# Optimization experiments

Hardware: AMD Instinct MI355X
Metric: run time of the kernel (lower is better)

## Reference

```python
import jax, jax.numpy as jnp
import numpy as np


def _dequantize_and_unpack(packed, scales):
    """packed: [d_out, d_in//2] int8, each byte holds two 4-bit nibbles.
    Returns [d_out, d_in] in scales.dtype, scaled per output row."""
    low = (packed & 15).astype(jnp.int8)
    high = (packed >> 4).astype(jnp.int8)  # arithmetic shift, like torch int8 >> 4
    low = jnp.where(low > 7, low - 16, low)
    high = jnp.where(high > 7, high - 16, high)
    # interleave: even cols = high nibble, odd cols = low nibble
    w = jnp.stack([high, low], axis=-1).reshape(packed.shape[0], -1)
    return w.astype(scales.dtype) * scales


def setup_inputs() -> dict:
    key = jax.random.key(0)
    ks = jax.random.split(key, 7)
    d = 4096
    N = 4096
    x = jax.random.normal(ks[0], (N, d), dtype=jnp.float32)
    fc1_weights_packed = jax.random.randint(ks[1], (2 * d, d // 2), -8, 7, dtype=jnp.int32).astype(jnp.int8)
    fc1_scales = (jax.random.normal(ks[2], (2 * d, 1), dtype=jnp.float32) * 0.02).astype(jnp.float16)
    fc1_bias = jax.random.normal(ks[3], (2 * d,), dtype=jnp.float32)
    fc2_weights_packed = jax.random.randint(ks[4], (d, d), -8, 7, dtype=jnp.int32).astype(jnp.int8)
    fc2_scales = (jax.random.normal(ks[5], (d, 1), dtype=jnp.float32) * 0.02).astype(jnp.float16)
    fc2_bias = jax.random.normal(ks[6], (d,), dtype=jnp.float32)
    return {
        "x": x,
        "fc1_weights_packed": fc1_weights_packed,
        "fc1_scales": fc1_scales,
        "fc1_bias": fc1_bias,
        "fc2_weights_packed": fc2_weights_packed,
        "fc2_scales": fc2_scales,
        "fc2_bias": fc2_bias,
    }


def reference(x, fc1_weights_packed, fc1_scales, fc1_bias,
              fc2_weights_packed, fc2_scales, fc2_bias):
    # fc1: dequantize to [2d, d], linear, relu
    w1 = _dequantize_and_unpack(fc1_weights_packed, fc1_scales).astype(x.dtype)
    h = jax.nn.relu(jnp.dot(x, w1.T) + fc1_bias)
    # fc2: dequantize to [d, 2d], linear
    w2 = _dequantize_and_unpack(fc2_weights_packed, fc2_scales).astype(x.dtype)
    return jnp.dot(h, w2.T) + fc2_bias
```

## Files before the change

kernel.cpp:

```cpp
#include <hip/hip_runtime.h>
#include <hip/hip_fp16.h>
#include <stdint.h>


typedef __attribute__((ext_vector_type(4)))  int i32x4;
typedef __attribute__((ext_vector_type(16))) int i32x16;
typedef __attribute__((ext_vector_type(8))) _Float16 f16x8;

__device__ __forceinline__ void load_lds16(const void* g, void* l) {
    __builtin_amdgcn_global_load_lds(
        (__attribute__((address_space(1))) void*)(void*)g,
        (__attribute__((address_space(3))) void*)(void*)l,
        16, 0, 0);
}

__device__ __forceinline__ float block_max(float m, int tid) {
    __shared__ float red[4];
#pragma unroll
    for (int off = 32; off; off >>= 1)
        m = fmaxf(m, __shfl_down(m, off, 64));
    if ((tid & 63) == 0) red[tid >> 6] = m;
    __syncthreads();
    m = fmaxf(fmaxf(red[0], red[1]), fmaxf(red[2], red[3]));
    __syncthreads();
    return m;
}

__global__ __launch_bounds__(256) void quant_x(
    const float* __restrict__ in, int* __restrict__ out,
    float* __restrict__ rscale, int ncols)
{
    const int tid = threadIdx.x;
    const int row = blockIdx.x;
    const float4* rp = (const float4*)(in + (size_t)row * ncols);
    const int nf4 = ncols / 4;
    float4 v[4];
    float m = 0.f;
#pragma unroll
    for (int k = 0; k < 4; ++k) {
        v[k] = rp[k * 256 + tid];
        m = fmaxf(m, fmaxf(fmaxf(fabsf(v[k].x), fabsf(v[k].y)),
                           fmaxf(fabsf(v[k].z), fabsf(v[k].w))));
    }
    m = block_max(m, tid);
    m = fmaxf(m, 1e-20f);
    const float inv = 127.f / m;
    if (tid == 0) rscale[row] = m / 127.f;
    int* orow = out + (size_t)row * nf4;
#pragma unroll
    for (int k = 0; k < 4; ++k) {
        int q0 = __float2int_rn(v[k].x * inv);
        int q1 = __float2int_rn(v[k].y * inv);
        int q2 = __float2int_rn(v[k].z * inv);
        int q3 = __float2int_rn(v[k].w * inv);
        orow[k * 256 + tid] = (q0 & 0xFF) | ((q1 & 0xFF) << 8) |
                              ((q2 & 0xFF) << 16) | ((q3 & 0xFF) << 24);
    }
}

__global__ __launch_bounds__(256) void quant_h(
    const _Float16* __restrict__ in, int2* __restrict__ out,
    float* __restrict__ rscale, int ncols)
{
    const int tid = threadIdx.x;
    const int row = blockIdx.x;
    const f16x8* rp = (const f16x8*)(in + (size_t)row * ncols);
    const int nv = ncols / 8;
    f16x8 v[4];
    float m = 0.f;
#pragma unroll
    for (int k = 0; k < 4; ++k) {
        v[k] = rp[k * 256 + tid];
#pragma unroll
        for (int e = 0; e < 8; ++e) m = fmaxf(m, (float)v[k][e]);
    }
    m = block_max(m, tid);
    m = fmaxf(m, 1e-20f);
    const float inv = 255.f / m;
    if (tid == 0) rscale[row] = m / 255.f;
    int2* orow = out + (size_t)row * nv;
#pragma unroll
    for (int k = 0; k < 4; ++k) {
        union { int8_t b[8]; int2 w; } u;
#pragma unroll
        for (int e = 0; e < 8; ++e) {
            int q = __float2int_rn((float)v[k][e] * inv);
            q = q < 0 ? 0 : (q > 255 ? 255 : q);
            u.b[e] = (int8_t)(q - 128);
        }
        orow[k * 256 + tid] = u.w;
    }
}

__global__ __launch_bounds__(256) void expand_int4_i8(
    const int4* __restrict__ packed, int2* __restrict__ out,
    int* __restrict__ wsum, int n_i4)
{
    const int tid = threadIdx.x;
    const int row = blockIdx.x;
    const int4* prow = packed + (size_t)row * n_i4;
    int2* orow = out + (size_t)row * n_i4;
    int sum = 0;
    for (int j = tid; j < n_i4; j += 256) {
        int4 p = prow[j];
        int vals[4] = {p.x, p.y, p.z, p.w};
        union { int8_t b[8]; int2 w; } u;
#pragma unroll
        for (int b = 0; b < 4; ++b) {
            int by = (int)(int8_t)(vals[b] & 0xFF);
            int hi = by >> 4;
            int lo = ((by & 15) ^ 8) - 8;
            u.b[2 * b] = (int8_t)hi;
            u.b[2 * b + 1] = (int8_t)lo;
            sum += hi + lo;
        }
        orow[j] = u.w;
    }
    __shared__ int sred[4];
#pragma unroll
    for (int off = 32; off; off >>= 1) sum += __shfl_down(sum, off, 64);
    if ((tid & 63) == 0) sred[tid >> 6] = sum;
    __syncthreads();
    if (tid == 0) wsum[row] = sred[0] + sred[1] + sred[2] + sred[3];
}

template <bool RELU, bool SHIFT, typename OutT>
__global__ __launch_bounds__(512, 2) void gemm_i8_256(
    const int8_t* __restrict__ A, const int8_t* __restrict__ B,
    OutT* __restrict__ C,
    const float* __restrict__ sa,
    const float* __restrict__ s,
    const float* __restrict__ bias,
    const int* __restrict__ wsum,
    int M, int N, int K)
{
    __shared__ alignas(16) char sA[2][256 * 128];
    __shared__ alignas(16) char sB[2][256 * 128];

    const int tid  = threadIdx.x;
    const int lane = tid & 63;
    const int wave = tid >> 6;
    const int wm = wave >> 2;
    const int wn = wave & 3;

    int bid = blockIdx.y * gridDim.x + blockIdx.x;
    const int xcd = bid & 7;
    const int idx = bid >> 3;
    const int cpx = gridDim.x >> 3;
    const int bx = xcd * cpx + idx / gridDim.y;
    const int by = idx % gridDim.y;
    const int bm = by * 256;
    const int bn = bx * 256;

    const int srow = tid >> 3;
    const int scol = ((tid & 7) ^ (srow & 7)) << 4;
    const int8_t* Ag = A + (size_t)(bm + srow) * K + scol;
    const int8_t* Bg = B + (size_t)(bn + srow) * K + scol;
    const size_t rK64 = (size_t)64 * K;
    const int ldst = tid * 16;

    auto stage_a = [&](int buf, int h, int kt) {
        const int8_t* g = Ag + (size_t)h * 128 * K + (size_t)kt * 128;
        char* l = &sA[buf][h * 16384 + ldst];
        load_lds16(g, l);
        load_lds16(g + rK64, l + 8192);
    };
    auto stage_b = [&](int buf, int h, int kt) {
        const int8_t* g = Bg + (size_t)h * 128 * K + (size_t)kt * 128;
        char* l = &sB[buf][h * 16384 + ldst];
        load_lds16(g, l);
        load_lds16(g + rK64, l + 8192);
    };

    const int l31 = lane & 31;
    const int kh  = lane >> 5;
    int coff[4];
#pragma unroll
    for (int ks = 0; ks < 4; ++ks)
        coff[ks] = (((ks * 2 + kh) ^ (l31 & 7)) << 4);
    int abase[4], bbase[2];
#pragma unroll
    for (int i = 0; i < 4; ++i) abase[i] = (wm * 128 + i * 32 + l31) * 128;
#pragma unroll
    for (int j = 0; j < 2; ++j) bbase[j] = (wn * 64 + j * 32 + l31) * 128;

    i32x16 acc[4][2] = {};
    const int NT = K >> 7;

    stage_a(0, 0, 0); stage_a(0, 1, 0);
    stage_b(0, 0, 0); stage_b(0, 1, 0);
    if (NT > 1) { stage_b(1, 0, 1); stage_b(1, 1, 1); }

#define MFMA_ROW(ri, AF)                                                   \
    do {                                                                   \
        __builtin_amdgcn_s_setprio(1);                                     \
        _Pragma("unroll")                                                  \
        for (int ks = 0; ks < 4; ++ks) {                                   \
            acc[ri][0] = __builtin_amdgcn_mfma_i32_32x32x32_i8(            \
                AF[ks], bf[0][ks], acc[ri][0], 0, 0, 0);                   \
            acc[ri][1] = __builtin_amdgcn_mfma_i32_32x32x32_i8(            \
                AF[ks], bf[1][ks], acc[ri][1], 0, 0, 0);                   \
        }                                                                  \
        __builtin_amdgcn_s_setprio(0);                                     \
    } while (0)

    for (int t = 0; t < NT; ++t) {
        const char* pA = sA[t & 1];
        const char* pB = sB[t & 1];
        if (t + 1 < NT) asm volatile("s_waitcnt vmcnt(4)" ::: "memory");
        else            asm volatile("s_waitcnt vmcnt(0)" ::: "memory");
        __builtin_amdgcn_s_barrier();
        __builtin_amdgcn_sched_barrier(0);

        i32x4 bf[2][4], afA[4], afB[4];
#pragma unroll
        for (int j = 0; j < 2; ++j)
#pragma unroll
            for (int ks = 0; ks < 4; ++ks)
                bf[j][ks] = *(const i32x4*)(pB + bbase[j] + coff[ks]);
#pragma unroll
        for (int ks = 0; ks < 4; ++ks)
            afA[ks] = *(const i32x4*)(pA + abase[0] + coff[ks]);
#pragma unroll
        for (int ks = 0; ks < 4; ++ks)
            afB[ks] = *(const i32x4*)(pA + abase[1] + coff[ks]);
        if (t + 1 < NT) stage_a((t + 1) & 1, 0, t + 1);
        __builtin_amdgcn_sched_barrier(0);
        asm volatile("s_waitcnt lgkmcnt(4)" ::: "memory");
        __builtin_amdgcn_sched_barrier(0);
        MFMA_ROW(0, afA);

#pragma unroll
        for (int ks = 0; ks < 4; ++ks)
            afA[ks] = *(const i32x4*)(pA + abase[2] + coff[ks]);
        if (t + 1 < NT) stage_a((t + 1) & 1, 1, t + 1);
        __builtin_amdgcn_sched_barrier(0);
        asm volatile("s_waitcnt lgkmcnt(4)" ::: "memory");
        __builtin_amdgcn_sched_barrier(0);
        MFMA_ROW(1, afB);

        __builtin_amdgcn_s_barrier();
        __builtin_amdgcn_sched_barrier(0);
#pragma unroll
        for (int ks = 0; ks < 4; ++ks)
            afB[ks] = *(const i32x4*)(pA + abase[3] + coff[ks]);
        if (t + 2 < NT) stage_b(t & 1, 0, t + 2);
        __builtin_amdgcn_sched_barrier(0);
        asm volatile("s_waitcnt lgkmcnt(4)" ::: "memory");
        __builtin_amdgcn_sched_barrier(0);
        MFMA_ROW(2, afA);

        if (t + 2 < NT) stage_b(t & 1, 1, t + 2);
        __builtin_amdgcn_sched_barrier(0);
        asm volatile("s_waitcnt lgkmcnt(0)" ::: "memory");
        __builtin_amdgcn_sched_barrier(0);
        MFMA_ROW(3, afB);
    }
#undef MFMA_ROW

#pragma unroll
    for (int j = 0; j < 2; ++j) {
        const int n  = bn + wn * 64 + j * 32 + l31;
        const float sc = s[n];
        const float bs = bias[n];
        const int shf = SHIFT ? 128 * wsum[n] : 0;
#pragma unroll
        for (int i = 0; i < 4; ++i) {
            const int mb = bm + wm * 128 + i * 32 + 4 * kh;
#pragma unroll
            for (int reg = 0; reg < 16; ++reg) {
                const int m = mb + (reg & 3) + 8 * (reg >> 2);
                float v = (float)(acc[i][j][reg] + shf) * sc * sa[m] + bs;
                if (RELU) v = v > 0.f ? v : 0.f;
                C[(size_t)m * N + n] = (OutT)v;
            }
        }
    }
}

extern "C" void kernel_launch(void* const* d_in, const int* in_sizes, int n_in,
                              void* d_out, int out_size, void* d_ws, size_t ws_size,
                              hipStream_t stream)
{
    const float* x   = (const float*)d_in[0];
    const int4*  w1p = (const int4*)d_in[1];
    const float* s1  = (const float*)d_in[2];
    const float* b1  = (const float*)d_in[3];
    const int4*  w2p = (const int4*)d_in[4];
    const float* s2  = (const float*)d_in[5];
    const float* b2  = (const float*)d_in[6];
    float* out = (float*)d_out;

    const int d    = in_sizes[6];
    const int d2   = in_sizes[3];
    const int Ntok = in_sizes[0] / d;

    char* ws = (char*)d_ws;
    int8_t*   xq = (int8_t*)ws;
    int8_t*   wq = (int8_t*)(ws + (size_t)Ntok * d);
    _Float16* hb = (_Float16*)(ws + (size_t)Ntok * d + (size_t)d2 * d);
    int8_t*   hq = (int8_t*)((char*)hb + (size_t)Ntok * d2 * 2);
    float*    sx = (float*)((char*)hq + (size_t)Ntok * d2);
    float*    sh = sx + Ntok;
    int*      wsum = (int*)(sh + Ntok);

    quant_x<<<Ntok, 256, 0, stream>>>(x, (int*)xq, sx, d);
    expand_int4_i8<<<d2, 256, 0, stream>>>(w1p, (int2*)wq, wsum, d / 8);
    {
        dim3 grid(d2 / 256, Ntok / 256);
        gemm_i8_256<true, false, _Float16><<<grid, 512, 0, stream>>>(
            xq, wq, hb, sx, s1, b1, nullptr, Ntok, d2, d);
    }
    quant_h<<<Ntok, 256, 0, stream>>>(hb, (int2*)hq, sh, d2);
    expand_int4_i8<<<d, 256, 0, stream>>>(w2p, (int2*)wq, wsum, d2 / 8);
    {
        dim3 grid(d / 256, Ntok / 256);
        gemm_i8_256<false, true, float><<<grid, 512, 0, stream>>>(
            hq, wq, out, sh, s2, b2, wsum, Ntok, d, d2);
    }
}
```

Baseline: 502.7 us.

## Reorder int8 GEMM main loop to iterate k-slices with double-buffered fragments

```diff
diff --git a/kernel.cpp b/kernel.cpp
--- a/kernel.cpp
+++ b/kernel.cpp
@@ -191,15 +191,25 @@
     stage_b(0, 0, 0); stage_b(0, 1, 0);
     if (NT > 1) { stage_b(1, 0, 1); stage_b(1, 1, 1); }
 
-#define MFMA_ROW(ri, AF)                                                   \
+#define READ_FRAGS(AF, BF, ks)                                             \
+    do {                                                                   \
+        _Pragma("unroll")                                                  \
+        for (int j = 0; j < 2; ++j)                                        \
+            BF[j] = *(const i32x4*)(pB + bbase[j] + coff[ks]);             \
+        _Pragma("unroll")                                                  \
+        for (int i = 0; i < 4; ++i)                                        \
+            AF[i] = *(const i32x4*)(pA + abase[i] + coff[ks]);             \
+    } while (0)
+
+#define MFMA8(AF, BF)                                                      \
     do {                                                                   \
         __builtin_amdgcn_s_setprio(1);                                     \
         _Pragma("unroll")                                                  \
-        for (int ks = 0; ks < 4; ++ks) {                                   \
-            acc[ri][0] = __builtin_amdgcn_mfma_i32_32x32x32_i8(            \
-                AF[ks], bf[0][ks], acc[ri][0], 0, 0, 0);                   \
-            acc[ri][1] = __builtin_amdgcn_mfma_i32_32x32x32_i8(            \
-                AF[ks], bf[1][ks], acc[ri][1], 0, 0, 0);                   \
+        for (int i = 0; i < 4; ++i) {                                      \
+            acc[i][0] = __builtin_amdgcn_mfma_i32_32x32x32_i8(             \
+                AF[i], BF[0], acc[i][0], 0, 0, 0);                         \
+            acc[i][1] = __builtin_amdgcn_mfma_i32_32x32x32_i8(             \
+                AF[i], BF[1], acc[i][1], 0, 0, 0);                         \
         }                                                                  \
         __builtin_amdgcn_s_setprio(0);                                     \
     } while (0)
@@ -212,51 +222,40 @@
         __builtin_amdgcn_s_barrier();
         __builtin_amdgcn_sched_barrier(0);
 
-        i32x4 bf[2][4], afA[4], afB[4];
-#pragma unroll
-        for (int j = 0; j < 2; ++j)
-#pragma unroll
-            for (int ks = 0; ks < 4; ++ks)
-                bf[j][ks] = *(const i32x4*)(pB + bbase[j] + coff[ks]);
-#pragma unroll
-        for (int ks = 0; ks < 4; ++ks)
-            afA[ks] = *(const i32x4*)(pA + abase[0] + coff[ks]);
-#pragma unroll
-        for (int ks = 0; ks < 4; ++ks)
-            afB[ks] = *(const i32x4*)(pA + abase[1] + coff[ks]);
-        if (t + 1 < NT) stage_a((t + 1) & 1, 0, t + 1);
-        __builtin_amdgcn_sched_barrier(0);
-        asm volatile("s_waitcnt lgkmcnt(4)" ::: "memory");
-        __builtin_amdgcn_sched_barrier(0);
-        MFMA_ROW(0, afA);
-
-#pragma unroll
-        for (int ks = 0; ks < 4; ++ks)
-            afA[ks] = *(const i32x4*)(pA + abase[2] + coff[ks]);
-        if (t + 1 < NT) stage_a((t + 1) & 1, 1, t + 1);
-        __builtin_amdgcn_sched_barrier(0);
-        asm volatile("s_waitcnt lgkmcnt(4)" ::: "memory");
-        __builtin_amdgcn_sched_barrier(0);
-        MFMA_ROW(1, afB);
-
+        i32x4 afX[4], bfX[2], afY[4], bfY[2];
+        READ_FRAGS(afX, bfX, 0);
+        if (t + 1 < NT) { stage_a((t + 1) & 1, 0, t + 1);
+                          stage_a((t + 1) & 1, 1, t + 1); }
+        __builtin_amdgcn_sched_barrier(0);
+
+        READ_FRAGS(afY, bfY, 1);
+        __builtin_amdgcn_sched_barrier(0);
+        asm volatile("s_waitcnt lgkmcnt(6)" ::: "memory");
+        __builtin_amdgcn_sched_barrier(0);
+        MFMA8(afX, bfX);
+
+        READ_FRAGS(afX, bfX, 2);
+        __builtin_amdgcn_sched_barrier(0);
+        asm volatile("s_waitcnt lgkmcnt(6)" ::: "memory");
+        __builtin_amdgcn_sched_barrier(0);
+        MFMA8(afY, bfY);
+
+        READ_FRAGS(afY, bfY, 3);
+        __builtin_amdgcn_sched_barrier(0);
+        asm volatile("s_waitcnt lgkmcnt(6)" ::: "memory");
+        __builtin_amdgcn_sched_barrier(0);
+        MFMA8(afX, bfX);
+
+        asm volatile("s_waitcnt lgkmcnt(0)" ::: "memory");
+        __builtin_amdgcn_sched_barrier(0);
         __builtin_amdgcn_s_barrier();
-        __builtin_amdgcn_sched_barrier(0);
-#pragma unroll
-        for (int ks = 0; ks < 4; ++ks)
-            afB[ks] = *(const i32x4*)(pA + abase[3] + coff[ks]);
-        if (t + 2 < NT) stage_b(t & 1, 0, t + 2);
-        __builtin_amdgcn_sched_barrier(0);
-        asm volatile("s_waitcnt lgkmcnt(4)" ::: "memory");
-        __builtin_amdgcn_sched_barrier(0);
-        MFMA_ROW(2, afA);
-
-        if (t + 2 < NT) stage_b(t & 1, 1, t + 2);
-        __builtin_amdgcn_sched_barrier(0);
-        asm volatile("s_waitcnt lgkmcnt(0)" ::: "memory");
-        __builtin_amdgcn_sched_barrier(0);
-        MFMA_ROW(3, afB);
-    }
-#undef MFMA_ROW
+        if (t + 2 < NT) { stage_b(t & 1, 0, t + 2);
+                          stage_b(t & 1, 1, t + 2); }
+        __builtin_amdgcn_sched_barrier(0);
+        MFMA8(afY, bfY);
+    }
+#undef READ_FRAGS
+#undef MFMA8
 
 #pragma unroll
     for (int j = 0; j < 2; ++j) {
```

After: 505.5 us. About the same (+0.6%).
